# Performance work log

Measured on AMD Instinct MI355X. Metric: run time of the kernel, lower is better.

Reference implementation:

```python
import jax, jax.numpy as jnp
import numpy as np

EPS = 1e-5

def _ln(x):
    # LayerNorm over last dim, no affine (elementwise_affine=False), biased variance
    mu = jnp.mean(x, axis=-1, keepdims=True)
    var = jnp.mean(jnp.square(x - mu), axis=-1, keepdims=True)
    return (x - mu) / jnp.sqrt(var + EPS)

def setup_inputs() -> dict:
    key = jax.random.key(0)
    B, I, H = 32768, 512, 512
    ks = jax.random.split(key, 12)
    std = 1.0 / np.sqrt(H)
    u = lambda k, shape: jax.random.uniform(k, shape, jnp.float32, -std, std)
    return {
        "x": jax.random.normal(ks[0], (B, I), jnp.float32),
        "h": jax.random.normal(ks[1], (B, H), jnp.float32),
        "W_i2h": u(ks[2], (I, 2 * H)),
        "b_i2h": u(ks[3], (2 * H,)),
        "W_h2h": u(ks[4], (H, 2 * H)),
        "b_h2h": u(ks[5], (2 * H,)),
        "W_hatW": u(ks[6], (I, H)),
        "b_hatW": u(ks[7], (H,)),
        "W_hatU": u(ks[8], (H, H)),
        "b_hatU": u(ks[9], (H,)),
    }

def reference(x, h, W_i2h, b_i2h, W_h2h, b_h2h, W_hatW, b_hatW, W_hatU, b_hatU):
    H = W_hatU.shape[0]
    i2h = _ln(x @ W_i2h + b_i2h)          # [B, 2H]
    h2h = _ln(h @ W_h2h + b_h2h)          # [B, 2H]
    gates = jax.nn.sigmoid(i2h + h2h)
    z_t = gates[:, :H]
    r_t = gates[:, -H:]
    h_hat_first = _ln(x @ W_hatW + b_hatW)  # [B, H]
    h_hat_last = _ln(h @ W_hatU + b_hatU)   # [B, H]
    h_hat = jnp.tanh(h_hat_first + r_t * h_hat_last)
    h_t = (1.0 - z_t) * h + z_t * h_hat
    return h_t
```

## Files before the change

kernel.cpp:

```cpp
#include <hip/hip_runtime.h>
#include <stdint.h>

typedef unsigned short u16;
typedef __attribute__((ext_vector_type(8))) short short8;
typedef __attribute__((ext_vector_type(4))) short short4v;
typedef __attribute__((ext_vector_type(4))) float f4;
typedef __attribute__((ext_vector_type(4))) float f32x4;

static __device__ __forceinline__ u16 f2b(float f) {
  union { float f; uint32_t u; } c; c.f = f;
  return (u16)((c.u + 0x7FFFu + ((c.u >> 16) & 1u)) >> 16);
}
static __device__ __forceinline__ float b2f(u16 s) {
  union { uint32_t u; float f; } c; c.u = ((uint32_t)s) << 16; return c.f;
}

__global__ __launch_bounds__(256) void cvt_kernel(const float* __restrict__ x,
                                                  const float* __restrict__ h,
                                                  u16* __restrict__ Ab) {
  const size_t half = (size_t)32768 * 512;
  size_t tid = (size_t)blockIdx.x * blockDim.x + threadIdx.x;
  size_t nth = (size_t)gridDim.x * blockDim.x;
  size_t total8 = (half * 2) >> 3;
  for (size_t t = tid; t < total8; t += nth) {
    size_t e = t << 3;
    const float* src = (e < half) ? (x + e) : (h + (e - half));
    f4 v0 = *(const f4*)src;
    f4 v1 = *(const f4*)(src + 4);
    short8 o;
    o[0] = (short)f2b(v0[0]); o[1] = (short)f2b(v0[1]);
    o[2] = (short)f2b(v0[2]); o[3] = (short)f2b(v0[3]);
    o[4] = (short)f2b(v1[0]); o[5] = (short)f2b(v1[1]);
    o[6] = (short)f2b(v1[2]); o[7] = (short)f2b(v1[3]);
    *(short8*)(Ab + e) = o;
  }
}

__global__ __launch_bounds__(256) void transpose_cat(const float* __restrict__ srcA,
                                                     const float* __restrict__ srcB,
                                                     u16* __restrict__ dst,
                                                     int NA, int NB) {
  __shared__ float t[32][33];
  int n0 = blockIdx.x * 32, k0 = blockIdx.y * 32;
  int tx = threadIdx.x, ty = threadIdx.y;
  const float* src; int strideN, nb;
  if (n0 < NA) { src = srcA; strideN = NA; nb = n0; }
  else         { src = srcB; strideN = NB; nb = n0 - NA; }
#pragma unroll
  for (int i = 0; i < 4; ++i) {
    int k = k0 + ty + i * 8;
    t[tx][ty + i * 8] = src[(size_t)k * strideN + nb + tx];
  }
  __syncthreads();
#pragma unroll
  for (int i = 0; i < 4; ++i) {
    int n = ty + i * 8;
    dst[(size_t)(n0 + n) * 512 + k0 + tx] = f2b(t[n][tx]);
  }
}

__global__ __launch_bounds__(256, 2) void gemm_kernel(
    const u16* __restrict__ Ab, const u16* __restrict__ WxT,
    const u16* __restrict__ WhT, u16* __restrict__ Cb,
    int rowStartX, int rowStartH, int tilesPerHalf) {
  __shared__ u16 As[128 * 64];
  __shared__ u16 Bs[128 * 64];

  int nwg = gridDim.x;
  int bid = blockIdx.x;
  int swz = (bid & 7) * (nwg >> 3) + (bid >> 3);
  int mb = swz / 12, nb = swz - mb * 12;
  size_t m0;
  const u16* Wt;
  if (mb < tilesPerHalf) { m0 = (size_t)rowStartX + (size_t)mb * 128; Wt = WxT; }
  else { m0 = (size_t)rowStartH + (size_t)(mb - tilesPerHalf) * 128; Wt = WhT; }
  int crow0 = mb * 128;
  int n0 = nb * 128;

  int tid = threadIdx.x, lane = tid & 63, wv = tid >> 6;
  int wm = wv >> 1, wn = wv & 1;
  int l15 = lane & 15, l4 = lane >> 4, l7 = lane & 7;

  f32x4 acc[4][4] = {};

  int sRow = lane >> 3;
  int g = (lane & 7) ^ sRow;

  for (int kt = 0; kt < 8; ++kt) {
    int k0 = kt << 6;
#pragma unroll
    for (int i = 0; i < 4; ++i) {
      int chunk = wv * 4 + i;
      int rowg = chunk * 8 + sRow;
      const u16* srcA = Ab + (m0 + rowg) * 512 + (k0 + g * 8);
      const u16* srcB = Wt + (size_t)(n0 + rowg) * 512 + (k0 + g * 8);
      __builtin_amdgcn_global_load_lds(
          (const __attribute__((address_space(1))) void*)srcA,
          (__attribute__((address_space(3))) void*)(As + chunk * 512), 16, 0, 0);
      __builtin_amdgcn_global_load_lds(
          (const __attribute__((address_space(1))) void*)srcB,
          (__attribute__((address_space(3))) void*)(Bs + chunk * 512), 16, 0, 0);
    }
    __syncthreads();
#pragma unroll
    for (int ks = 0; ks < 2; ++ks) {
      short8 af[4], bf[4];
#pragma unroll
      for (int mr = 0; mr < 4; ++mr) {
        int r = wm * 64 + mr * 16 + l15;
        int slot = (ks * 4 + l4) ^ l7;
        af[mr] = *(const short8*)(As + r * 64 + slot * 8);
      }
#pragma unroll
      for (int nr = 0; nr < 4; ++nr) {
        int r = wn * 64 + nr * 16 + l15;
        int slot = (ks * 4 + l4) ^ l7;
        bf[nr] = *(const short8*)(Bs + r * 64 + slot * 8);
      }
#pragma unroll
      for (int mr = 0; mr < 4; ++mr)
#pragma unroll
        for (int nr = 0; nr < 4; ++nr)
          acc[mr][nr] = __builtin_amdgcn_mfma_f32_16x16x32_bf16(
              bf[nr], af[mr], acc[mr][nr], 0, 0, 0);
    }
    __syncthreads();
  }

#pragma unroll
  for (int mr = 0; mr < 4; ++mr) {
    int m = crow0 + wm * 64 + mr * 16 + l15;
#pragma unroll
    for (int nr = 0; nr < 4; ++nr) {
      int n = n0 + wn * 64 + nr * 16 + l4 * 4;
      short4v o;
      o[0] = (short)f2b(acc[mr][nr][0]);
      o[1] = (short)f2b(acc[mr][nr][1]);
      o[2] = (short)f2b(acc[mr][nr][2]);
      o[3] = (short)f2b(acc[mr][nr][3]);
      *(short4v*)(Cb + (size_t)m * 1536 + n) = o;
    }
  }
}

__global__ __launch_bounds__(256) void epi_kernel(
    const u16* __restrict__ Cb, const float* __restrict__ h,
    const float* __restrict__ b_i2h, const float* __restrict__ b_h2h,
    const float* __restrict__ b_hatW, const float* __restrict__ b_hatU,
    float* __restrict__ out, int mBase, int BC) {
  int wv = threadIdx.x >> 6;
  int lane = threadIdx.x & 63;
  int mLocal = blockIdx.x * 4 + wv;
  size_t mGlob = (size_t)mBase + mLocal;
  const u16* Ar = Cb + (size_t)mLocal * 1536;
  const u16* Br = Cb + ((size_t)BC + mLocal) * 1536;
  int j0 = lane * 8;

  float a[3][8], b[3][8];
#pragma unroll
  for (int c = 0; c < 3; ++c) {
    short8 va = *(const short8*)(Ar + c * 512 + j0);
    short8 vb = *(const short8*)(Br + c * 512 + j0);
    const float* biasA = (c == 0) ? (b_i2h + j0) : (c == 1) ? (b_i2h + 512 + j0) : (b_hatW + j0);
    const float* biasB = (c == 0) ? (b_h2h + j0) : (c == 1) ? (b_h2h + 512 + j0) : (b_hatU + j0);
    f4 ba0 = *(const f4*)biasA, ba1 = *(const f4*)(biasA + 4);
    f4 bb0 = *(const f4*)biasB, bb1 = *(const f4*)(biasB + 4);
#pragma unroll
    for (int j = 0; j < 4; ++j) {
      a[c][j]     = b2f((u16)va[j])     + ba0[j];
      a[c][j + 4] = b2f((u16)va[j + 4]) + ba1[j];
      b[c][j]     = b2f((u16)vb[j])     + bb0[j];
      b[c][j + 4] = b2f((u16)vb[j + 4]) + bb1[j];
    }
  }

  float s1a = 0, q1a = 0, s2a = 0, q2a = 0, s1b = 0, q1b = 0, s2b = 0, q2b = 0;
#pragma unroll
  for (int j = 0; j < 8; ++j) {
    s1a += a[0][j] + a[1][j]; q1a += a[0][j] * a[0][j] + a[1][j] * a[1][j];
    s2a += a[2][j];           q2a += a[2][j] * a[2][j];
    s1b += b[0][j] + b[1][j]; q1b += b[0][j] * b[0][j] + b[1][j] * b[1][j];
    s2b += b[2][j];           q2b += b[2][j] * b[2][j];
  }
#pragma unroll
  for (int off = 32; off > 0; off >>= 1) {
    s1a += __shfl_xor(s1a, off); q1a += __shfl_xor(q1a, off);
    s2a += __shfl_xor(s2a, off); q2a += __shfl_xor(q2a, off);
    s1b += __shfl_xor(s1b, off); q1b += __shfl_xor(q1b, off);
    s2b += __shfl_xor(s2b, off); q2b += __shfl_xor(q2b, off);
  }
  const float inv1 = 1.0f / 1024.0f, inv2 = 1.0f / 512.0f, eps = 1e-5f;
  float mu1a = s1a * inv1, mu2a = s2a * inv2, mu1b = s1b * inv1, mu2b = s2b * inv2;
  float rs1a = rsqrtf(q1a * inv1 - mu1a * mu1a + eps);
  float rs2a = rsqrtf(q2a * inv2 - mu2a * mu2a + eps);
  float rs1b = rsqrtf(q1b * inv1 - mu1b * mu1b + eps);
  float rs2b = rsqrtf(q2b * inv2 - mu2b * mu2b + eps);

  const float* hrow = h + mGlob * 512 + j0;
  f4 h0 = *(const f4*)hrow, h1 = *(const f4*)(hrow + 4);
  f4 o0, o1;
#pragma unroll
  for (int j = 0; j < 8; ++j) {
    float zs  = (a[0][j] - mu1a) * rs1a + (b[0][j] - mu1b) * rs1b;
    float rsg = (a[1][j] - mu1a) * rs1a + (b[1][j] - mu1b) * rs1b;
    float z = 1.0f / (1.0f + __expf(-zs));
    float r = 1.0f / (1.0f + __expf(-rsg));
    float hh = tanhf((a[2][j] - mu2a) * rs2a + r * ((b[2][j] - mu2b) * rs2b));
    float hv = (j < 4) ? h0[j] : h1[j - 4];
    float o = hv + z * (hh - hv);
    if (j < 4) o0[j] = o; else o1[j - 4] = o;
  }
  *(f4*)(out + mGlob * 512 + j0) = o0;
  *(f4*)(out + mGlob * 512 + j0 + 4) = o1;
}

extern "C" void kernel_launch(void* const* d_in, const int* in_sizes, int n_in,
                              void* d_out, int out_size, void* d_ws, size_t ws_size,
                              hipStream_t stream) {
  const float* x      = (const float*)d_in[0];
  const float* h      = (const float*)d_in[1];
  const float* W_i2h  = (const float*)d_in[2];
  const float* b_i2h  = (const float*)d_in[3];
  const float* W_h2h  = (const float*)d_in[4];
  const float* b_h2h  = (const float*)d_in[5];
  const float* W_hatW = (const float*)d_in[6];
  const float* b_hatW = (const float*)d_in[7];
  const float* W_hatU = (const float*)d_in[8];
  const float* b_hatU = (const float*)d_in[9];
  float* out = (float*)d_out;

  u16* WxT = (u16*)d_ws;
  u16* WhT = WxT + (size_t)1536 * 512;
  u16* Ab  = WhT + (size_t)1536 * 512;
  u16* Cb  = Ab + (size_t)65536 * 512;

  size_t fixedElems = (size_t)2 * 1536 * 512 + (size_t)65536 * 512;
  int chunks = 1;
  for (;;) {
    size_t need = (fixedElems + (size_t)2 * (32768 / chunks) * 1536) * sizeof(u16);
    if (need <= ws_size || chunks >= 128) break;
    chunks <<= 1;
  }
  int BC = 32768 / chunks;
  int tph = BC / 128;
  int nwg = 2 * tph * 12;

  cvt_kernel<<<2048, 256, 0, stream>>>(x, h, Ab);
  transpose_cat<<<dim3(48, 16), dim3(32, 8), 0, stream>>>(W_i2h, W_hatW, WxT, 1024, 512);
  transpose_cat<<<dim3(48, 16), dim3(32, 8), 0, stream>>>(W_h2h, W_hatU, WhT, 1024, 512);
  for (int cc = 0; cc < chunks; ++cc) {
    gemm_kernel<<<nwg, 256, 0, stream>>>(Ab, WxT, WhT, Cb,
                                         cc * BC, 32768 + cc * BC, tph);
    epi_kernel<<<BC / 4, 256, 0, stream>>>(Cb, h, b_i2h, b_h2h, b_hatW, b_hatU,
                                           out, cc * BC, BC);
  }
}
```

Measured before the change: 241.5 us.

## Enlarge GEMM tiles to 256x256 with 4-stage async LDS pipeline

Rewrites the bf16 GEMM to use 256x256 output tiles with 512 threads (8 waves), a K-step of 32, and a 4-buffer ring of global-to-LDS loads kept three stages ahead, synchronized with explicit vmcnt waits. It also raises MFMA priority during compute and uses a new XOR swizzle matched to 32-wide rows. The aim is to raise data reuse per tile and overlap memory loads with MFMA work. In exchange it uses 128 KB of LDS per block and more accumulator registers, which may limit occupancy, and it produces fewer workgroups.

```diff
diff --git a/kernel.cpp b/kernel.cpp
--- a/kernel.cpp
+++ b/kernel.cpp
@@ -59,77 +59,88 @@
   }
 }
 
-__global__ __launch_bounds__(256, 2) void gemm_kernel(
+#define AS1 __attribute__((address_space(1)))
+#define AS3 __attribute__((address_space(3)))
+
+__global__ __launch_bounds__(512, 2) void gemm_kernel(
     const u16* __restrict__ Ab, const u16* __restrict__ WxT,
     const u16* __restrict__ WhT, u16* __restrict__ Cb,
     int rowStartX, int rowStartH, int tilesPerHalf) {
-  __shared__ u16 As[128 * 64];
-  __shared__ u16 Bs[128 * 64];
-
-  int nwg = gridDim.x;
-  int bid = blockIdx.x;
-  int swz = (bid & 7) * (nwg >> 3) + (bid >> 3);
-  int mb = swz / 12, nb = swz - mb * 12;
-  size_t m0;
-  const u16* Wt;
-  if (mb < tilesPerHalf) { m0 = (size_t)rowStartX + (size_t)mb * 128; Wt = WxT; }
-  else { m0 = (size_t)rowStartH + (size_t)(mb - tilesPerHalf) * 128; Wt = WhT; }
-  int crow0 = mb * 128;
-  int n0 = nb * 128;
+  __shared__ u16 lds[65536];
 
   int tid = threadIdx.x, lane = tid & 63, wv = tid >> 6;
-  int wm = wv >> 1, wn = wv & 1;
-  int l15 = lane & 15, l4 = lane >> 4, l7 = lane & 7;
-
-  f32x4 acc[4][4] = {};
-
-  int sRow = lane >> 3;
-  int g = (lane & 7) ^ sRow;
-
-  for (int kt = 0; kt < 8; ++kt) {
-    int k0 = kt << 6;
-#pragma unroll
-    for (int i = 0; i < 4; ++i) {
-      int chunk = wv * 4 + i;
-      int rowg = chunk * 8 + sRow;
-      const u16* srcA = Ab + (m0 + rowg) * 512 + (k0 + g * 8);
-      const u16* srcB = Wt + (size_t)(n0 + rowg) * 512 + (k0 + g * 8);
-      __builtin_amdgcn_global_load_lds(
-          (const __attribute__((address_space(1))) void*)srcA,
-          (__attribute__((address_space(3))) void*)(As + chunk * 512), 16, 0, 0);
-      __builtin_amdgcn_global_load_lds(
-          (const __attribute__((address_space(1))) void*)srcB,
-          (__attribute__((address_space(3))) void*)(Bs + chunk * 512), 16, 0, 0);
+  int wm = wv >> 2, wn = wv & 3;
+  int l15 = lane & 15, l4 = lane >> 4;
+
+  int nwg = gridDim.x, bid = blockIdx.x;
+  int swz = (nwg & 7) ? bid : ((bid & 7) * (nwg >> 3) + (bid >> 3));
+  int mb = swz / 6, nb = swz - mb * 6;
+  size_t m0; const u16* Wt;
+  if (mb < tilesPerHalf) { m0 = (size_t)rowStartX + (size_t)mb * 256; Wt = WxT; }
+  else { m0 = (size_t)rowStartH + (size_t)(mb - tilesPerHalf) * 256; Wt = WhT; }
+  int crow0 = mb * 256, n0 = nb * 256;
+
+  int idx0 = wv * 128 + lane, idx1 = idx0 + 64;
+  int r0 = idx0 >> 2, c0 = (idx0 & 3) ^ ((r0 ^ (r0 >> 2)) & 3);
+  int r1 = idx1 >> 2, c1 = (idx1 & 3) ^ ((r1 ^ (r1 >> 2)) & 3);
+  const u16* sA0 = Ab + (m0 + r0) * 512 + c0 * 8;
+  const u16* sA1 = Ab + (m0 + r1) * 512 + c1 * 8;
+  const u16* sB0 = Wt + (size_t)(n0 + r0) * 512 + c0 * 8;
+  const u16* sB1 = Wt + (size_t)(n0 + r1) * 512 + c1 * 8;
+  int dOffA = wv * 1024;
+
+  int gl = (l15 ^ (l15 >> 2)) & 3;
+  int slot = l4 ^ gl;
+  int aOff = (wm * 128 + l15) * 32 + slot * 8;
+  int bOff = 8192 + (wn * 64 + l15) * 32 + slot * 8;
+
+  f32x4 acc[8][4] = {};
+
+#define STG(t) do { \
+    u16* _b = lds + (((t) & 3) << 14); \
+    __builtin_amdgcn_global_load_lds((const AS1 void*)(sA0 + (t) * 32), (AS3 void*)(_b + dOffA), 16, 0, 0); \
+    __builtin_amdgcn_global_load_lds((const AS1 void*)(sA1 + (t) * 32), (AS3 void*)(_b + dOffA + 512), 16, 0, 0); \
+    __builtin_amdgcn_global_load_lds((const AS1 void*)(sB0 + (t) * 32), (AS3 void*)(_b + 8192 + dOffA), 16, 0, 0); \
+    __builtin_amdgcn_global_load_lds((const AS1 void*)(sB1 + (t) * 32), (AS3 void*)(_b + 8192 + dOffA + 512), 16, 0, 0); \
+  } while (0)
+
+  STG(0); STG(1); STG(2);
+  asm volatile("s_waitcnt vmcnt(8)" ::: "memory");
+  __builtin_amdgcn_sched_barrier(0);
+  __builtin_amdgcn_s_barrier();
+  __builtin_amdgcn_sched_barrier(0);
+
+#pragma unroll
+  for (int t = 0; t < 16; ++t) {
+    const u16* buf = lds + ((t & 3) << 14);
+    if (t < 13) STG(t + 3);
+    short8 bfr[4], afr[8];
+#pragma unroll
+    for (int nr = 0; nr < 4; ++nr) bfr[nr] = *(const short8*)(buf + bOff + nr * 512);
+#pragma unroll
+    for (int mr = 0; mr < 8; ++mr) afr[mr] = *(const short8*)(buf + aOff + mr * 512);
+    __builtin_amdgcn_s_setprio(1);
+#pragma unroll
+    for (int mr = 0; mr < 8; ++mr)
+#pragma unroll
+      for (int nr = 0; nr < 4; ++nr)
+        acc[mr][nr] = __builtin_amdgcn_mfma_f32_16x16x32_bf16(
+            bfr[nr], afr[mr], acc[mr][nr], 0, 0, 0);
+    __builtin_amdgcn_s_setprio(0);
+    if (t < 13)       { asm volatile("s_waitcnt vmcnt(8)" ::: "memory"); }
+    else if (t == 13) { asm volatile("s_waitcnt vmcnt(4)" ::: "memory"); }
+    else if (t == 14) { asm volatile("s_waitcnt vmcnt(0)" ::: "memory"); }
+    if (t < 15) {
+      __builtin_amdgcn_sched_barrier(0);
+      __builtin_amdgcn_s_barrier();
+      __builtin_amdgcn_sched_barrier(0);
     }
-    __syncthreads();
-#pragma unroll
-    for (int ks = 0; ks < 2; ++ks) {
-      short8 af[4], bf[4];
-#pragma unroll
-      for (int mr = 0; mr < 4; ++mr) {
-        int r = wm * 64 + mr * 16 + l15;
-        int slot = (ks * 4 + l4) ^ l7;
-        af[mr] = *(const short8*)(As + r * 64 + slot * 8);
-      }
-#pragma unroll
-      for (int nr = 0; nr < 4; ++nr) {
-        int r = wn * 64 + nr * 16 + l15;
-        int slot = (ks * 4 + l4) ^ l7;
-        bf[nr] = *(const short8*)(Bs + r * 64 + slot * 8);
-      }
-#pragma unroll
-      for (int mr = 0; mr < 4; ++mr)
-#pragma unroll
-        for (int nr = 0; nr < 4; ++nr)
-          acc[mr][nr] = __builtin_amdgcn_mfma_f32_16x16x32_bf16(
-              bf[nr], af[mr], acc[mr][nr], 0, 0, 0);
-    }
-    __syncthreads();
-  }
-
-#pragma unroll
-  for (int mr = 0; mr < 4; ++mr) {
-    int m = crow0 + wm * 64 + mr * 16 + l15;
+  }
+#undef STG
+
+#pragma unroll
+  for (int mr = 0; mr < 8; ++mr) {
+    int m = crow0 + wm * 128 + mr * 16 + l15;
 #pragma unroll
     for (int nr = 0; nr < 4; ++nr) {
       int n = n0 + wn * 64 + nr * 16 + l4 * 4;
@@ -242,14 +253,14 @@
     chunks <<= 1;
   }
   int BC = 32768 / chunks;
-  int tph = BC / 128;
-  int nwg = 2 * tph * 12;
+  int tph = BC / 256;
+  int nwg = 2 * tph * 6;
 
   cvt_kernel<<<2048, 256, 0, stream>>>(x, h, Ab);
   transpose_cat<<<dim3(48, 16), dim3(32, 8), 0, stream>>>(W_i2h, W_hatW, WxT, 1024, 512);
   transpose_cat<<<dim3(48, 16), dim3(32, 8), 0, stream>>>(W_h2h, W_hatU, WhT, 1024, 512);
   for (int cc = 0; cc < chunks; ++cc) {
-    gemm_kernel<<<nwg, 256, 0, stream>>>(Ab, WxT, WhT, Cb,
+    gemm_kernel<<<nwg, 512, 0, stream>>>(Ab, WxT, WhT, Cb,
                                          cc * BC, 32768 + cc * BC, tph);
     epi_kernel<<<BC / 4, 256, 0, stream>>>(Cb, h, b_i2h, b_h2h, b_hatW, b_hatU,
                                            out, cc * BC, BC);
```

Measured after the change: 251.0 us. 4.0% more time.

## Fuse fp32-to-bf16 input conversion into GEMM A-tile loading with register prefetch

Applied to the files above, without the earlier changes.

Drops the separate conversion kernel and has the GEMM load fp32 activations directly, converting to bf16 in registers before writing to swizzled LDS. Next k-tile A loads are issued before the current MFMA loop to overlap global latency. This removes a full read/write pass over the activations and the bf16 staging buffer, at the cost of reading twice the bytes for A per GEMM tile and higher register pressure; occupancy hint raised to 3.

```diff
diff --git a/kernel.cpp b/kernel.cpp
--- a/kernel.cpp
+++ b/kernel.cpp
@@ -1,4 +1,5 @@
 #include <hip/hip_runtime.h>
+#include <hip/hip_bf16.h>
 #include <stdint.h>
 
 typedef unsigned short u16;
@@ -14,26 +15,9 @@
 static __device__ __forceinline__ float b2f(u16 s) {
   union { uint32_t u; float f; } c; c.u = ((uint32_t)s) << 16; return c.f;
 }
-
-__global__ __launch_bounds__(256) void cvt_kernel(const float* __restrict__ x,
-                                                  const float* __restrict__ h,
-                                                  u16* __restrict__ Ab) {
-  const size_t half = (size_t)32768 * 512;
-  size_t tid = (size_t)blockIdx.x * blockDim.x + threadIdx.x;
-  size_t nth = (size_t)gridDim.x * blockDim.x;
-  size_t total8 = (half * 2) >> 3;
-  for (size_t t = tid; t < total8; t += nth) {
-    size_t e = t << 3;
-    const float* src = (e < half) ? (x + e) : (h + (e - half));
-    f4 v0 = *(const f4*)src;
-    f4 v1 = *(const f4*)(src + 4);
-    short8 o;
-    o[0] = (short)f2b(v0[0]); o[1] = (short)f2b(v0[1]);
-    o[2] = (short)f2b(v0[2]); o[3] = (short)f2b(v0[3]);
-    o[4] = (short)f2b(v1[0]); o[5] = (short)f2b(v1[1]);
-    o[6] = (short)f2b(v1[2]); o[7] = (short)f2b(v1[3]);
-    *(short8*)(Ab + e) = o;
-  }
+static __device__ __forceinline__ uint32_t pk2(float lo, float hi) {
+  __hip_bfloat162 b = __float22bfloat162_rn(make_float2(lo, hi));
+  union { __hip_bfloat162 b; uint32_t u; } c; c.b = b; return c.u;
 }
 
 __global__ __launch_bounds__(256) void transpose_cat(const float* __restrict__ srcA,
@@ -59,10 +43,13 @@
   }
 }
 
-__global__ __launch_bounds__(256, 2) void gemm_kernel(
-    const u16* __restrict__ Ab, const u16* __restrict__ WxT,
-    const u16* __restrict__ WhT, u16* __restrict__ Cb,
-    int rowStartX, int rowStartH, int tilesPerHalf) {
+#define AS1 __attribute__((address_space(1)))
+#define AS3 __attribute__((address_space(3)))
+
+__global__ __launch_bounds__(256, 3) void gemm_kernel(
+    const float* __restrict__ X, const float* __restrict__ Hm,
+    const u16* __restrict__ WxT, const u16* __restrict__ WhT,
+    u16* __restrict__ Cb, int rowStart, int tilesPerHalf) {
   __shared__ u16 As[128 * 64];
   __shared__ u16 Bs[128 * 64];
 
@@ -70,10 +57,13 @@
   int bid = blockIdx.x;
   int swz = (bid & 7) * (nwg >> 3) + (bid >> 3);
   int mb = swz / 12, nb = swz - mb * 12;
-  size_t m0;
+  const float* Asrc;
   const u16* Wt;
-  if (mb < tilesPerHalf) { m0 = (size_t)rowStartX + (size_t)mb * 128; Wt = WxT; }
-  else { m0 = (size_t)rowStartH + (size_t)(mb - tilesPerHalf) * 128; Wt = WhT; }
+  if (mb < tilesPerHalf) {
+    Asrc = X + (size_t)(rowStart + mb * 128) * 512; Wt = WxT;
+  } else {
+    Asrc = Hm + (size_t)(rowStart + (mb - tilesPerHalf) * 128) * 512; Wt = WhT;
+  }
   int crow0 = mb * 128;
   int n0 = nb * 128;
 
@@ -83,40 +73,63 @@
 
   f32x4 acc[4][4] = {};
 
+  int arow = tid >> 4;
+  int ak4 = (tid & 15) * 4;
+  int s8 = ak4 >> 3;
+  int ahalf = (ak4 & 7) ? 4 : 0;
+  const float* abase = Asrc + (size_t)arow * 512 + ak4;
+  u16* awr = As + arow * 64 + ((s8 ^ (arow & 7)) << 3) + ahalf;
+
   int sRow = lane >> 3;
   int g = (lane & 7) ^ sRow;
+  const u16* bbase = Wt + (size_t)(n0 + sRow) * 512 + g * 8;
+
+  int slot0 = ((0 * 4 + l4) ^ l7) * 8;
+  int slot1 = ((1 * 4 + l4) ^ l7) * 8;
+  int aOff = (wm * 64 + l15) * 64;
+  int bOff = (wn * 64 + l15) * 64;
+
+  f4 va[8];
+
+#define LOADA(kt) do { \
+    _Pragma("unroll") \
+    for (int p = 0; p < 8; ++p) \
+      va[p] = *(const f4*)(abase + (size_t)(p * 16) * 512 + (kt) * 64); \
+  } while (0)
+
+#define WRITEA() do { \
+    _Pragma("unroll") \
+    for (int p = 0; p < 8; ++p) { \
+      uint2 w; w.x = pk2(va[p][0], va[p][1]); w.y = pk2(va[p][2], va[p][3]); \
+      *(uint2*)(awr + p * 1024) = w; \
+    } \
+  } while (0)
+
+#define STGB(kt) do { \
+    _Pragma("unroll") \
+    for (int i = 0; i < 4; ++i) { \
+      int chunk = wv * 4 + i; \
+      __builtin_amdgcn_global_load_lds( \
+          (const AS1 void*)(bbase + (size_t)(chunk * 8) * 512 + (kt) * 64), \
+          (AS3 void*)(Bs + chunk * 512), 16, 0, 0); \
+    } \
+  } while (0)
+
+  LOADA(0);
+  STGB(0);
+  WRITEA();
+  __syncthreads();
 
   for (int kt = 0; kt < 8; ++kt) {
-    int k0 = kt << 6;
-#pragma unroll
-    for (int i = 0; i < 4; ++i) {
-      int chunk = wv * 4 + i;
-      int rowg = chunk * 8 + sRow;
-      const u16* srcA = Ab + (m0 + rowg) * 512 + (k0 + g * 8);
-      const u16* srcB = Wt + (size_t)(n0 + rowg) * 512 + (k0 + g * 8);
-      __builtin_amdgcn_global_load_lds(
-          (const __attribute__((address_space(1))) void*)srcA,
-          (__attribute__((address_space(3))) void*)(As + chunk * 512), 16, 0, 0);
-      __builtin_amdgcn_global_load_lds(
-          (const __attribute__((address_space(1))) void*)srcB,
-          (__attribute__((address_space(3))) void*)(Bs + chunk * 512), 16, 0, 0);
-    }
-    __syncthreads();
+    if (kt < 7) LOADA(kt + 1);
+    short8 af[4], bf[4];
 #pragma unroll
     for (int ks = 0; ks < 2; ++ks) {
-      short8 af[4], bf[4];
-#pragma unroll
-      for (int mr = 0; mr < 4; ++mr) {
-        int r = wm * 64 + mr * 16 + l15;
-        int slot = (ks * 4 + l4) ^ l7;
-        af[mr] = *(const short8*)(As + r * 64 + slot * 8);
-      }
-#pragma unroll
-      for (int nr = 0; nr < 4; ++nr) {
-        int r = wn * 64 + nr * 16 + l15;
-        int slot = (ks * 4 + l4) ^ l7;
-        bf[nr] = *(const short8*)(Bs + r * 64 + slot * 8);
-      }
+      int sl = ks ? slot1 : slot0;
+#pragma unroll
+      for (int mr = 0; mr < 4; ++mr) af[mr] = *(const short8*)(As + aOff + mr * 1024 + sl);
+#pragma unroll
+      for (int nr = 0; nr < 4; ++nr) bf[nr] = *(const short8*)(Bs + bOff + nr * 1024 + sl);
 #pragma unroll
       for (int mr = 0; mr < 4; ++mr)
 #pragma unroll
@@ -125,7 +138,15 @@
               bf[nr], af[mr], acc[mr][nr], 0, 0, 0);
     }
     __syncthreads();
-  }
+    if (kt < 7) {
+      STGB(kt + 1);
+      WRITEA();
+      __syncthreads();
+    }
+  }
+#undef LOADA
+#undef WRITEA
+#undef STGB
 
 #pragma unroll
   for (int mr = 0; mr < 4; ++mr) {
@@ -231,10 +252,9 @@
 
   u16* WxT = (u16*)d_ws;
   u16* WhT = WxT + (size_t)1536 * 512;
-  u16* Ab  = WhT + (size_t)1536 * 512;
-  u16* Cb  = Ab + (size_t)65536 * 512;
-
-  size_t fixedElems = (size_t)2 * 1536 * 512 + (size_t)65536 * 512;
+  u16* Cb  = WhT + (size_t)1536 * 512;
+
+  size_t fixedElems = (size_t)2 * 1536 * 512;
   int chunks = 1;
   for (;;) {
     size_t need = (fixedElems + (size_t)2 * (32768 / chunks) * 1536) * sizeof(u16);
@@ -245,12 +265,10 @@
   int tph = BC / 128;
   int nwg = 2 * tph * 12;
 
-  cvt_kernel<<<2048, 256, 0, stream>>>(x, h, Ab);
   transpose_cat<<<dim3(48, 16), dim3(32, 8), 0, stream>>>(W_i2h, W_hatW, WxT, 1024, 512);
   transpose_cat<<<dim3(48, 16), dim3(32, 8), 0, stream>>>(W_h2h, W_hatU, WhT, 1024, 512);
   for (int cc = 0; cc < chunks; ++cc) {
-    gemm_kernel<<<nwg, 256, 0, stream>>>(Ab, WxT, WhT, Cb,
-                                         cc * BC, 32768 + cc * BC, tph);
+    gemm_kernel<<<nwg, 256, 0, stream>>>(x, h, WxT, WhT, Cb, cc * BC, tph);
     epi_kernel<<<BC / 4, 256, 0, stream>>>(Cb, h, b_i2h, b_h2h, b_hatW, b_hatU,
                                            out, cc * BC, BC);
   }
```

Measured after the change: 270.5 us. 1.12x slower.
